# Optimization experiments

Hardware: AMD Instinct MI355X
Metric: run time of the kernel (lower is better)

The kernel has to match this reference:

```python
import jax, jax.numpy as jnp
import numpy as np

D_K = 128


def setup_inputs() -> dict:
    key = jax.random.key(0)
    k = jax.random.split(key, 5)
    B, H, H_KV, S_Q, S_PAST, D = 2, 16, 4, 1024, 1024, D_K
    return {
        "Q": jax.random.normal(k[0], (B, H, S_Q, D), dtype=jnp.float32),
        "K": jax.random.normal(k[1], (B, H, S_Q, D), dtype=jnp.float32),
        "V": jax.random.normal(k[2], (B, H, S_Q, D), dtype=jnp.float32),
        "past_key": jax.random.normal(k[3], (B, H_KV, S_PAST, D), dtype=jnp.float32),
        "past_value": jax.random.normal(k[4], (B, H_KV, S_PAST, D), dtype=jnp.float32),
    }


def reference(Q, K, V, past_key, past_value):
    B, H, S_q, D = Q.shape
    H_kv = past_key.shape[1]
    n_groups = H // H_kv
    scale = 1.0 / jnp.sqrt(jnp.float32(D_K))

    # expand_grouped_kv: [B,H_kv,S,D] -> [B,H_kv,G,S,D] -> [B,H,S,D] == repeat along heads
    pk = jnp.repeat(past_key, n_groups, axis=1)
    pv = jnp.repeat(past_value, n_groups, axis=1)
    K_full = jnp.concatenate([pk, K], axis=2)   # [B,H,S_k,D]
    V_full = jnp.concatenate([pv, V], axis=2)
    present_key = K_full[:, ::n_groups]         # [B,H_kv,S_present,D]
    present_value = V_full[:, ::n_groups]

    S_k = K_full.shape[2]
    scores = jnp.einsum("bhqd,bhkd->bhqk", Q, K_full) * scale  # [B,H,S_q,S_k]
    start = S_k - S_q
    # torch.tril(ones(S_q,S_k), diagonal=start): key j visible iff j <= q + start
    causal = jnp.arange(S_k)[None, :] <= (jnp.arange(S_q)[:, None] + start)
    scores = jnp.where(causal[None, None], scores, jnp.float32(-jnp.inf))
    attn = jax.nn.softmax(scores, axis=-1)
    out = jnp.einsum("bhqk,bhkd->bhqd", attn, V_full)
    return out, present_key, present_value
```

## Files before the change

kernel.cpp:

```cpp
#include <hip/hip_runtime.h>
#include <hip/hip_bf16.h>

#define B_    2
#define H_    16
#define HKV_  4
#define SQ_   1024
#define SP_   1024
#define SK_   2048
#define D_    128
#define QBLK  64
#define KVBLK 64

typedef __attribute__((ext_vector_type(8))) __bf16 bf16x8;
typedef __attribute__((ext_vector_type(4))) __bf16 bf16x4;
typedef __attribute__((ext_vector_type(4))) float  f32x4;

__device__ inline __bf16 f2bf(float f) { return (__bf16)f; }

__global__ __launch_bounds__(256, 2)
void attn_fwd_kernel(const float* __restrict__ Q, const float* __restrict__ Kin,
                     const float* __restrict__ Vin, const float* __restrict__ PK,
                     const float* __restrict__ PV, float* __restrict__ Out)
{
    __shared__ __align__(16) __bf16 Klds[KVBLK * D_];
    __shared__ __align__(16) __bf16 Vlds[D_ * KVBLK];
    __shared__ __align__(16) __bf16 Plds[4 * 16 * KVBLK];

    const int tid  = threadIdx.x;
    const int lane = tid & 63;
    const int w    = tid >> 6;
    const int lr   = lane & 15;
    const int lg   = lane >> 4;

    const int qt = blockIdx.x;
    const int h  = blockIdx.y;
    const int b  = blockIdx.z;
    const int q0w = qt * QBLK + w * 16;

    const float scale_l2e = 0.08838834764831845f * 1.4426950408889634f;

    bf16x8 qf[4];
    {
        const float* qsrc = Q + (((size_t)b*H_ + h)*SQ_ + q0w + lr)*(size_t)D_ + lg*8;
        #pragma unroll
        for (int c = 0; c < 4; ++c) {
            f32x4 a0 = *(const f32x4*)(qsrc + c*32);
            f32x4 a1 = *(const f32x4*)(qsrc + c*32 + 4);
            bf16x8 f;
            #pragma unroll
            for (int j = 0; j < 4; ++j) {
                f[j]   = f2bf(a0[j] * scale_l2e);
                f[j+4] = f2bf(a1[j] * scale_l2e);
            }
            qf[c] = f;
        }
    }

    f32x4 o[8];
    #pragma unroll
    for (int i = 0; i < 8; ++i) o[i] = (f32x4){0.f,0.f,0.f,0.f};
    float m_r = -1e30f, l_r = 0.f;

    const int ntiles = qt + 17;

    const size_t pk_base = (((size_t)b*HKV_ + (h>>2))*SP_)*(size_t)D_;
    const size_t kn_base = (((size_t)b*H_   + h     )*SQ_)*(size_t)D_;

    f32x4 kreg[4][2], vreg[2][4];

    {
        const float* ks = PK + pk_base;
        #pragma unroll
        for (int i = 0; i < 4; ++i) {
            int idx = i*256 + tid, row = idx >> 4, c8 = idx & 15;
            kreg[i][0] = *(const f32x4*)(ks + row*D_ + c8*8);
            kreg[i][1] = *(const f32x4*)(ks + row*D_ + c8*8 + 4);
        }
        const float* vs = PV + pk_base;
        #pragma unroll
        for (int i = 0; i < 2; ++i) {
            int blk = i*256 + tid, bk = blk & 15, bd = blk >> 4;
            #pragma unroll
            for (int kk = 0; kk < 4; ++kk)
                vreg[i][kk] = *(const f32x4*)(vs + (4*bk+kk)*D_ + bd*4);
        }
    }

    for (int kt = 0; kt < ntiles; ++kt) {
        const int k0 = kt * KVBLK;
        __syncthreads();

        #pragma unroll
        for (int i = 0; i < 4; ++i) {
            int idx = i*256 + tid, row = idx >> 4, c8 = idx & 15;
            bf16x8 f;
            #pragma unroll
            for (int j = 0; j < 4; ++j) {
                f[j]   = f2bf(kreg[i][0][j]);
                f[j+4] = f2bf(kreg[i][1][j]);
            }
            int off = (row*256 + c8*16) ^ ((row & 7) << 4);
            *(bf16x8*)((char*)Klds + off) = f;
        }
        #pragma unroll
        for (int i = 0; i < 2; ++i) {
            int blk = i*256 + tid, bk = blk & 15, bd = blk >> 4;
            #pragma unroll
            for (int j = 0; j < 4; ++j) {
                int d = 4*bd + j;
                bf16x4 t;
                t[0]=f2bf(vreg[i][0][j]); t[1]=f2bf(vreg[i][1][j]);
                t[2]=f2bf(vreg[i][2][j]); t[3]=f2bf(vreg[i][3][j]);
                int off = (d*128 + bk*8) ^ ((d & 7) << 4);
                *(bf16x4*)((char*)Vlds + off) = t;
            }
        }
        __syncthreads();

        if (kt + 1 < ntiles) {
            const int k1 = k0 + KVBLK;
            const float* ks = (k1 < SP_) ? PK + pk_base + (size_t)k1*D_
                                         : Kin + kn_base + (size_t)(k1 - SP_)*D_;
            #pragma unroll
            for (int i = 0; i < 4; ++i) {
                int idx = i*256 + tid, row = idx >> 4, c8 = idx & 15;
                kreg[i][0] = *(const f32x4*)(ks + row*D_ + c8*8);
                kreg[i][1] = *(const f32x4*)(ks + row*D_ + c8*8 + 4);
            }
            const float* vs = (k1 < SP_) ? PV + pk_base + (size_t)k1*D_
                                         : Vin + kn_base + (size_t)(k1 - SP_)*D_;
            #pragma unroll
            for (int i = 0; i < 2; ++i) {
                int blk = i*256 + tid, bk = blk & 15, bd = blk >> 4;
                #pragma unroll
                for (int kk = 0; kk < 4; ++kk)
                    vreg[i][kk] = *(const f32x4*)(vs + (4*bk+kk)*D_ + bd*4);
            }
        }

        f32x4 s[4];
        #pragma unroll
        for (int n = 0; n < 4; ++n) s[n] = (f32x4){0.f,0.f,0.f,0.f};
        #pragma unroll
        for (int n = 0; n < 4; ++n) {
            #pragma unroll
            for (int c = 0; c < 4; ++c) {
                int off = ((n*16 + lr)*256 + c*64 + lg*16) ^ ((lr & 7) << 4);
                bf16x8 kf = *(const bf16x8*)((char*)Klds + off);
                s[n] = __builtin_amdgcn_mfma_f32_16x16x32_bf16(kf, qf[c], s[n], 0, 0, 0);
            }
        }

        float p[16];
        const bool needmask = (k0 + KVBLK - 1) > (q0w + SP_);
        if (needmask) {
            const int qv = q0w + lr + SP_;
            #pragma unroll
            for (int n = 0; n < 4; ++n)
                #pragma unroll
                for (int r = 0; r < 4; ++r) {
                    int kg = k0 + n*16 + lg*4 + r;
                    p[n*4+r] = (kg <= qv) ? s[n][r] : -1e30f;
                }
        } else {
            #pragma unroll
            for (int n = 0; n < 4; ++n)
                #pragma unroll
                for (int r = 0; r < 4; ++r) p[n*4+r] = s[n][r];
        }

        float mx = p[0];
        #pragma unroll
        for (int i = 1; i < 16; ++i) mx = fmaxf(mx, p[i]);
        mx = fmaxf(mx, __shfl_xor(mx, 16));
        mx = fmaxf(mx, __shfl_xor(mx, 32));
        float mnew  = fmaxf(m_r, mx);
        float alpha = exp2f(m_r - mnew);
        m_r = mnew;
        float psum = 0.f;
        #pragma unroll
        for (int i = 0; i < 16; ++i) { p[i] = exp2f(p[i] - mnew); psum += p[i]; }
        psum += __shfl_xor(psum, 16);
        psum += __shfl_xor(psum, 32);
        l_r = l_r * alpha + psum;
        #pragma unroll
        for (int dt = 0; dt < 8; ++dt) {
            o[dt][0] *= alpha; o[dt][1] *= alpha;
            o[dt][2] *= alpha; o[dt][3] *= alpha;
        }

        char* Pw = (char*)Plds + w*2048;
        #pragma unroll
        for (int n = 0; n < 4; ++n) {
            bf16x4 t;
            t[0]=f2bf(p[n*4+0]); t[1]=f2bf(p[n*4+1]);
            t[2]=f2bf(p[n*4+2]); t[3]=f2bf(p[n*4+3]);
            int off = (lr*128 + n*32 + lg*8) ^ ((lr & 7) << 4);
            *(bf16x4*)(Pw + off) = t;
        }

        #pragma unroll
        for (int kk = 0; kk < 2; ++kk) {
            int poff = (lr*128 + kk*64 + lg*16) ^ ((lr & 7) << 4);
            bf16x8 pa = *(const bf16x8*)(Pw + poff);
            #pragma unroll
            for (int dt = 0; dt < 8; ++dt) {
                int voff = ((dt*16 + lr)*128 + kk*64 + lg*16) ^ ((lr & 7) << 4);
                bf16x8 vf = *(const bf16x8*)((char*)Vlds + voff);
                o[dt] = __builtin_amdgcn_mfma_f32_16x16x32_bf16(vf, pa, o[dt], 0, 0, 0);
            }
        }
    }

    float inv = 1.0f / l_r;
    float* orow = Out + (((size_t)b*H_ + h)*SQ_ + q0w + lr)*(size_t)D_;
    #pragma unroll
    for (int dt = 0; dt < 8; ++dt) {
        f32x4 st;
        st[0]=o[dt][0]*inv; st[1]=o[dt][1]*inv;
        st[2]=o[dt][2]*inv; st[3]=o[dt][3]*inv;
        *(f32x4*)(orow + dt*16 + lg*4) = st;
    }
}

__global__ __launch_bounds__(256)
void copy_present_kernel(const float* __restrict__ Kin, const float* __restrict__ Vin,
                         const float* __restrict__ PK,  const float* __restrict__ PV,
                         float* __restrict__ opk, float* __restrict__ opv)
{
    const int n4 = B_*HKV_*SK_*(D_/4);
    int idx = blockIdx.x*256 + threadIdx.x;
    bool isV = false;
    if (idx >= n4) { idx -= n4; isV = true; }
    int d4 = idx & 31;
    int s  = (idx >> 5) & (SK_-1);
    int bg = idx >> 16;
    int bb = bg >> 2, g = bg & 3;
    const float* srcp;
    if (s < SP_)
        srcp = (isV ? PV : PK) + (((size_t)bg)*SP_ + s)*(size_t)D_ + d4*4;
    else
        srcp = (isV ? Vin : Kin) + (((size_t)(bb*H_ + 4*g))*SQ_ + (s - SP_))*(size_t)D_ + d4*4;
    float4 v = *(const float4*)srcp;
    float* dstp = (isV ? opv : opk) + (size_t)idx*4;
    *(float4*)dstp = v;
}

extern "C" void kernel_launch(void* const* d_in, const int* in_sizes, int n_in,
                              void* d_out, int out_size, void* d_ws, size_t ws_size,
                              hipStream_t stream) {
    const float* Q   = (const float*)d_in[0];
    const float* K   = (const float*)d_in[1];
    const float* V   = (const float*)d_in[2];
    const float* PK  = (const float*)d_in[3];
    const float* PV  = (const float*)d_in[4];
    float* out = (float*)d_out;
    float* opk = out + (size_t)B_*H_*SQ_*D_;
    float* opv = opk + (size_t)B_*HKV_*SK_*D_;

    dim3 agrid(SQ_/QBLK, H_, B_);
    attn_fwd_kernel<<<agrid, 256, 0, stream>>>(Q, K, V, PK, PV, out);

    int copyblocks = (2 * B_*HKV_*SK_*(D_/4)) / 256;
    copy_present_kernel<<<copyblocks, 256, 0, stream>>>(K, V, PK, PV, opk, opv);
}
```

Before: 98.93 us.

## Fuse present-KV copy into attention kernel, double-buffer LDS, lazy softmax rescale

Merges the present-key/value copy into the attention launch through an extra grid column of copy blocks, which removes the second kernel launch. It also double-buffers the K/V LDS tiles so only one barrier is needed per tile, reverses the q-tile order for batch 1 to balance load, and raises wave priority around the MFMA sections. The softmax now skips rescaling unless the running max grows by more than a threshold, which saves exp and multiply work. The cost is more LDS per block, which may lower occupancy, and copy blocks that compete with attention blocks for bandwidth.

After: 123.5 us. 24.9% more time.

```diff
diff --git a/kernel.cpp b/kernel.cpp
--- a/kernel.cpp
+++ b/kernel.cpp
@@ -18,24 +18,47 @@
 __device__ inline __bf16 f2bf(float f) { return (__bf16)f; }
 
 __global__ __launch_bounds__(256, 2)
-void attn_fwd_kernel(const float* __restrict__ Q, const float* __restrict__ Kin,
-                     const float* __restrict__ Vin, const float* __restrict__ PK,
-                     const float* __restrict__ PV, float* __restrict__ Out)
+void attn_fused_kernel(const float* __restrict__ Q, const float* __restrict__ Kin,
+                       const float* __restrict__ Vin, const float* __restrict__ PK,
+                       const float* __restrict__ PV, float* __restrict__ Out,
+                       float* __restrict__ opk, float* __restrict__ opv)
 {
-    __shared__ __align__(16) __bf16 Klds[KVBLK * D_];
-    __shared__ __align__(16) __bf16 Vlds[D_ * KVBLK];
+    __shared__ __align__(16) __bf16 Klds[2][KVBLK * D_];
+    __shared__ __align__(16) __bf16 Vlds[2][D_ * KVBLK];
     __shared__ __align__(16) __bf16 Plds[4 * 16 * KVBLK];
 
-    const int tid  = threadIdx.x;
+    const int tid = threadIdx.x;
+    const int qtx = blockIdx.x;
+    const int h   = blockIdx.y;
+    const int b   = blockIdx.z;
+
+    if (qtx == 16) {
+        const int n4 = B_*HKV_*SK_*(D_/4);
+        const int sid = b*16 + h;
+        #pragma unroll 4
+        for (int i = 0; i < 128; ++i) {
+            int idx = sid*32768 + i*256 + tid;
+            bool isV = idx >= n4;
+            int id2 = isV ? idx - n4 : idx;
+            int d4 = id2 & 31;
+            int s  = (id2 >> 5) & (SK_-1);
+            int bg = id2 >> 16;
+            int bb = bg >> 2, g = bg & 3;
+            const float* srcp = (s < SP_)
+                ? (isV ? PV : PK) + (((size_t)bg)*SP_ + s)*(size_t)D_ + d4*4
+                : (isV ? Vin : Kin) + (((size_t)(bb*H_ + 4*g))*SQ_ + (s - SP_))*(size_t)D_ + d4*4;
+            float4 v = *(const float4*)srcp;
+            *(float4*)((isV ? opv : opk) + (size_t)id2*4) = v;
+        }
+        return;
+    }
+
+    const int qt = b ? (15 - qtx) : qtx;
     const int lane = tid & 63;
     const int w    = tid >> 6;
     const int lr   = lane & 15;
     const int lg   = lane >> 4;
-
-    const int qt = blockIdx.x;
-    const int h  = blockIdx.y;
-    const int b  = blockIdx.z;
-    const int q0w = qt * QBLK + w * 16;
+    const int q0w  = qt * QBLK + w * 16;
 
     const float scale_l2e = 0.08838834764831845f * 1.4426950408889634f;
 
@@ -61,22 +84,19 @@
     for (int i = 0; i < 8; ++i) o[i] = (f32x4){0.f,0.f,0.f,0.f};
     float m_r = -1e30f, l_r = 0.f;
 
-    const int ntiles = qt + 17;
-
+    const int nt = qt + 17;
     const size_t pk_base = (((size_t)b*HKV_ + (h>>2))*SP_)*(size_t)D_;
     const size_t kn_base = (((size_t)b*H_   + h     )*SQ_)*(size_t)D_;
 
     f32x4 kreg[4][2], vreg[2][4];
 
-    {
-        const float* ks = PK + pk_base;
+    auto loadKV = [&](const float* ks, const float* vs) {
         #pragma unroll
         for (int i = 0; i < 4; ++i) {
             int idx = i*256 + tid, row = idx >> 4, c8 = idx & 15;
             kreg[i][0] = *(const f32x4*)(ks + row*D_ + c8*8);
             kreg[i][1] = *(const f32x4*)(ks + row*D_ + c8*8 + 4);
         }
-        const float* vs = PV + pk_base;
         #pragma unroll
         for (int i = 0; i < 2; ++i) {
             int blk = i*256 + tid, bk = blk & 15, bd = blk >> 4;
@@ -84,12 +104,8 @@
             for (int kk = 0; kk < 4; ++kk)
                 vreg[i][kk] = *(const f32x4*)(vs + (4*bk+kk)*D_ + bd*4);
         }
-    }
-
-    for (int kt = 0; kt < ntiles; ++kt) {
-        const int k0 = kt * KVBLK;
-        __syncthreads();
-
+    };
+    auto writeKV = [&](int buf) {
         #pragma unroll
         for (int i = 0; i < 4; ++i) {
             int idx = i*256 + tid, row = idx >> 4, c8 = idx & 15;
@@ -100,7 +116,7 @@
                 f[j+4] = f2bf(kreg[i][1][j]);
             }
             int off = (row*256 + c8*16) ^ ((row & 7) << 4);
-            *(bf16x8*)((char*)Klds + off) = f;
+            *(bf16x8*)((char*)Klds[buf] + off) = f;
         }
         #pragma unroll
         for (int i = 0; i < 2; ++i) {
@@ -112,49 +128,49 @@
                 t[0]=f2bf(vreg[i][0][j]); t[1]=f2bf(vreg[i][1][j]);
                 t[2]=f2bf(vreg[i][2][j]); t[3]=f2bf(vreg[i][3][j]);
                 int off = (d*128 + bk*8) ^ ((d & 7) << 4);
-                *(bf16x4*)((char*)Vlds + off) = t;
-            }
-        }
-        __syncthreads();
-
-        if (kt + 1 < ntiles) {
-            const int k1 = k0 + KVBLK;
+                *(bf16x4*)((char*)Vlds[buf] + off) = t;
+            }
+        }
+    };
+
+    loadKV(PK + pk_base, PV + pk_base);
+    writeKV(0);
+    __syncthreads();
+
+    for (int kt = 0; kt < nt; ++kt) {
+        const int cur = kt & 1;
+
+        if (kt + 1 < nt) {
+            const int k1 = (kt + 1) * KVBLK;
             const float* ks = (k1 < SP_) ? PK + pk_base + (size_t)k1*D_
                                          : Kin + kn_base + (size_t)(k1 - SP_)*D_;
-            #pragma unroll
-            for (int i = 0; i < 4; ++i) {
-                int idx = i*256 + tid, row = idx >> 4, c8 = idx & 15;
-                kreg[i][0] = *(const f32x4*)(ks + row*D_ + c8*8);
-                kreg[i][1] = *(const f32x4*)(ks + row*D_ + c8*8 + 4);
-            }
             const float* vs = (k1 < SP_) ? PV + pk_base + (size_t)k1*D_
                                          : Vin + kn_base + (size_t)(k1 - SP_)*D_;
-            #pragma unroll
-            for (int i = 0; i < 2; ++i) {
-                int blk = i*256 + tid, bk = blk & 15, bd = blk >> 4;
-                #pragma unroll
-                for (int kk = 0; kk < 4; ++kk)
-                    vreg[i][kk] = *(const f32x4*)(vs + (4*bk+kk)*D_ + bd*4);
-            }
-        }
+            loadKV(ks, vs);
+        }
+
+        const char* Kb = (const char*)Klds[cur];
+        const char* Vb = (const char*)Vlds[cur];
 
         f32x4 s[4];
         #pragma unroll
         for (int n = 0; n < 4; ++n) s[n] = (f32x4){0.f,0.f,0.f,0.f};
+        __builtin_amdgcn_s_setprio(1);
         #pragma unroll
         for (int n = 0; n < 4; ++n) {
             #pragma unroll
             for (int c = 0; c < 4; ++c) {
                 int off = ((n*16 + lr)*256 + c*64 + lg*16) ^ ((lr & 7) << 4);
-                bf16x8 kf = *(const bf16x8*)((char*)Klds + off);
+                bf16x8 kf = *(const bf16x8*)(Kb + off);
                 s[n] = __builtin_amdgcn_mfma_f32_16x16x32_bf16(kf, qf[c], s[n], 0, 0, 0);
             }
         }
+        __builtin_amdgcn_s_setprio(0);
 
         float p[16];
-        const bool needmask = (k0 + KVBLK - 1) > (q0w + SP_);
-        if (needmask) {
+        if (kt == nt - 1) {
             const int qv = q0w + lr + SP_;
+            const int k0 = kt * KVBLK;
             #pragma unroll
             for (int n = 0; n < 4; ++n)
                 #pragma unroll
@@ -174,20 +190,23 @@
         for (int i = 1; i < 16; ++i) mx = fmaxf(mx, p[i]);
         mx = fmaxf(mx, __shfl_xor(mx, 16));
         mx = fmaxf(mx, __shfl_xor(mx, 32));
-        float mnew  = fmaxf(m_r, mx);
-        float alpha = exp2f(m_r - mnew);
-        m_r = mnew;
+        if (!__all(mx <= m_r + 8.0f)) {
+            float mnew  = fmaxf(m_r, mx);
+            float alpha = exp2f(m_r - mnew);
+            m_r = mnew;
+            l_r *= alpha;
+            #pragma unroll
+            for (int dt = 0; dt < 8; ++dt) {
+                o[dt][0] *= alpha; o[dt][1] *= alpha;
+                o[dt][2] *= alpha; o[dt][3] *= alpha;
+            }
+        }
         float psum = 0.f;
         #pragma unroll
-        for (int i = 0; i < 16; ++i) { p[i] = exp2f(p[i] - mnew); psum += p[i]; }
+        for (int i = 0; i < 16; ++i) { p[i] = exp2f(p[i] - m_r); psum += p[i]; }
         psum += __shfl_xor(psum, 16);
         psum += __shfl_xor(psum, 32);
-        l_r = l_r * alpha + psum;
-        #pragma unroll
-        for (int dt = 0; dt < 8; ++dt) {
-            o[dt][0] *= alpha; o[dt][1] *= alpha;
-            o[dt][2] *= alpha; o[dt][3] *= alpha;
-        }
+        l_r += psum;
 
         char* Pw = (char*)Plds + w*2048;
         #pragma unroll
@@ -199,6 +218,7 @@
             *(bf16x4*)(Pw + off) = t;
         }
 
+        __builtin_amdgcn_s_setprio(1);
         #pragma unroll
         for (int kk = 0; kk < 2; ++kk) {
             int poff = (lr*128 + kk*64 + lg*16) ^ ((lr & 7) << 4);
@@ -206,9 +226,15 @@
             #pragma unroll
             for (int dt = 0; dt < 8; ++dt) {
                 int voff = ((dt*16 + lr)*128 + kk*64 + lg*16) ^ ((lr & 7) << 4);
-                bf16x8 vf = *(const bf16x8*)((char*)Vlds + voff);
+                bf16x8 vf = *(const bf16x8*)(Vb + voff);
                 o[dt] = __builtin_amdgcn_mfma_f32_16x16x32_bf16(vf, pa, o[dt], 0, 0, 0);
             }
+        }
+        __builtin_amdgcn_s_setprio(0);
+
+        if (kt + 1 < nt) {
+            writeKV(cur ^ 1);
+            __syncthreads();
         }
     }
 
@@ -221,29 +247,6 @@
         st[2]=o[dt][2]*inv; st[3]=o[dt][3]*inv;
         *(f32x4*)(orow + dt*16 + lg*4) = st;
     }
-}
-
-__global__ __launch_bounds__(256)
-void copy_present_kernel(const float* __restrict__ Kin, const float* __restrict__ Vin,
-                         const float* __restrict__ PK,  const float* __restrict__ PV,
-                         float* __restrict__ opk, float* __restrict__ opv)
-{
-    const int n4 = B_*HKV_*SK_*(D_/4);
-    int idx = blockIdx.x*256 + threadIdx.x;
-    bool isV = false;
-    if (idx >= n4) { idx -= n4; isV = true; }
-    int d4 = idx & 31;
-    int s  = (idx >> 5) & (SK_-1);
-    int bg = idx >> 16;
-    int bb = bg >> 2, g = bg & 3;
-    const float* srcp;
-    if (s < SP_)
-        srcp = (isV ? PV : PK) + (((size_t)bg)*SP_ + s)*(size_t)D_ + d4*4;
-    else
-        srcp = (isV ? Vin : Kin) + (((size_t)(bb*H_ + 4*g))*SQ_ + (s - SP_))*(size_t)D_ + d4*4;
-    float4 v = *(const float4*)srcp;
-    float* dstp = (isV ? opv : opk) + (size_t)idx*4;
-    *(float4*)dstp = v;
 }
 
 extern "C" void kernel_launch(void* const* d_in, const int* in_sizes, int n_in,
@@ -258,9 +261,6 @@
     float* opk = out + (size_t)B_*H_*SQ_*D_;
     float* opv = opk + (size_t)B_*HKV_*SK_*D_;
 
-    dim3 agrid(SQ_/QBLK, H_, B_);
-    attn_fwd_kernel<<<agrid, 256, 0, stream>>>(Q, K, V, PK, PV, out);
-
-    int copyblocks = (2 * B_*HKV_*SK_*(D_/4)) / 256;
-    copy_present_kernel<<<copyblocks, 256, 0, stream>>>(K, V, PK, PV, opk, opv);
+    dim3 agrid(17, H_, B_);
+    attn_fused_kernel<<<agrid, 256, 0, stream>>>(Q, K, V, PK, PV, out, opk, opv);
 }
```
